# Optimization experiments

Measured on AMD Instinct MI355X. Metric: run time of the kernel, lower is better.

Reference implementation:

```python
import jax, jax.numpy as jnp
import numpy as np

N_NODES = 50000


def sage_conv(x, src, dst, Wl, bl, Wr):
    # mean-aggregate neighbor features: message from src -> dst
    msg = x[src]                                            # [E, d]
    agg = jax.ops.segment_sum(msg, dst, num_segments=N_NODES)
    deg = jax.ops.segment_sum(jnp.ones((src.shape[0],), x.dtype), dst,
                              num_segments=N_NODES)
    mean = agg / jnp.clip(deg, 1.0)[:, None]                # [N, d]
    # PyG SAGEConv: lin_l(mean) + lin_r(x); lin_l has bias, lin_r does not
    return mean @ Wl.T + bl + x @ Wr.T


def setup_inputs() -> dict:
    key = jax.random.key(0)
    ks = jax.random.split(key, 10)
    d_in, d_h = 128, 256
    E = 800000
    x = jax.random.normal(ks[0], (N_NODES, d_in), jnp.float32)
    edge_index = jax.random.randint(ks[1], (2, E), 0, N_NODES, jnp.int32)
    s = 0.05
    return {
        "x": x,
        "edge_index": edge_index,
        "W1_l": jax.random.normal(ks[2], (d_h, d_in), jnp.float32) * s,
        "b1": jax.random.normal(ks[3], (d_h,), jnp.float32) * s,
        "W1_r": jax.random.normal(ks[4], (d_h, d_in), jnp.float32) * s,
        "W2_l": jax.random.normal(ks[5], (d_h, d_h), jnp.float32) * s,
        "b2": jax.random.normal(ks[6], (d_h,), jnp.float32) * s,
        "W2_r": jax.random.normal(ks[7], (d_h, d_h), jnp.float32) * s,
        "head_w": jax.random.normal(ks[8], (1, d_h), jnp.float32) * s,
        "head_b": jax.random.normal(ks[9], (1,), jnp.float32) * s,
    }


def reference(x, edge_index, W1_l, b1, W1_r, W2_l, b2, W2_r, head_w, head_b):
    src, dst = edge_index[0], edge_index[1]
    h = jax.nn.relu(sage_conv(x, src, dst, W1_l, b1, W1_r))
    # dropout is identity in eval mode
    h = jax.nn.relu(sage_conv(h, src, dst, W2_l, b2, W2_r))
    out = h @ head_w.T + head_b                              # [N, 1]
    return out[:, 0]                                         # [N]
```

## Files before the change

kernel.cpp:

```cpp
#include <hip/hip_runtime.h>
#include <hip/hip_bf16.h>

#define D_IN 128
#define D_H  256

typedef __attribute__((ext_vector_type(8))) short short8;
typedef __attribute__((ext_vector_type(4))) float floatx4;

__device__ __forceinline__ unsigned short f2bf(float f) {
    __hip_bfloat16 h = __float2bfloat16(f);
    return *reinterpret_cast<unsigned short*>(&h);
}
__device__ __forceinline__ float bf2f(unsigned short s) {
    union { unsigned int u; float f; } v;
    v.u = ((unsigned int)s) << 16;
    return v.f;
}

__global__ void hist_conv_k(const int* __restrict__ dst, int* __restrict__ deg,
                            int* __restrict__ rank, int E,
                            const float* __restrict__ x, unsigned short* __restrict__ xb, int nx4,
                            const float* __restrict__ w1l, unsigned short* __restrict__ w1lb,
                            const float* __restrict__ w1r, unsigned short* __restrict__ w1rb, int nw14,
                            const float* __restrict__ w2l, unsigned short* __restrict__ w2lb,
                            const float* __restrict__ w2r, unsigned short* __restrict__ w2rb, int nw24) {
    if (blockIdx.x < 512) {
        for (int e = blockIdx.x * 256 + threadIdx.x; e < E; e += 512 * 256)
            rank[e] = atomicAdd(&deg[dst[e]], 1);
        return;
    }
    int i = (blockIdx.x - 512) * 256 + threadIdx.x;
    const float* s; unsigned short* d; int k;
    if (i < nx4) { s = x; d = xb; k = i; }
    else {
        i -= nx4;
        if (i < nw14) { s = w1l; d = w1lb; k = i; }
        else {
            i -= nw14;
            if (i < nw14) { s = w1r; d = w1rb; k = i; }
            else {
                i -= nw14;
                if (i < nw24) { s = w2l; d = w2lb; k = i; }
                else {
                    i -= nw24;
                    if (i >= nw24) return;
                    s = w2r; d = w2rb; k = i;
                }
            }
        }
    }
    float4 v = ((const float4*)s)[k];
    ushort4 u;
    u.x = f2bf(v.x); u.y = f2bf(v.y); u.z = f2bf(v.z); u.w = f2bf(v.w);
    ((ushort4*)d)[k] = u;
}

__global__ __launch_bounds__(256) void scan_part_k(const int* __restrict__ deg,
                                                   int* __restrict__ bsum, int n) {
    const int b = blockIdx.x, tid = threadIdx.x;
    const int base = b * 2048;
    const int lim = min(base + 2048, n);
    int s = 0;
    for (int i = base + tid; i < lim; i += 256) s += deg[i];
    __shared__ int red[256];
    red[tid] = s; __syncthreads();
    for (int off = 128; off > 0; off >>= 1) {
        if (tid < off) red[tid] += red[tid + off];
        __syncthreads();
    }
    if (tid == 0) bsum[b] = red[0];
}

__global__ __launch_bounds__(256) void scan_final_k(const int* __restrict__ deg,
                                                    const int* __restrict__ bsum,
                                                    int* __restrict__ row_ptr,
                                                    int n, int E) {
    const int b = blockIdx.x, tid = threadIdx.x;
    const int base = b * 2048;
    __shared__ int buf[2048];
    __shared__ int ts[256];
    __shared__ int blk_prefix;
    if (tid == 0) {
        int p = 0;
        for (int i = 0; i < b; ++i) p += bsum[i];
        blk_prefix = p;
    }
    for (int i = tid; i < 2048; i += 256)
        buf[i] = (base + i < n) ? deg[base + i] : 0;
    __syncthreads();
    int local[8];
    int s = 0;
#pragma unroll
    for (int j = 0; j < 8; ++j) { local[j] = s; s += buf[tid * 8 + j]; }
    ts[tid] = s; __syncthreads();
    for (int off = 1; off < 256; off <<= 1) {
        int v = (tid >= off) ? ts[tid - off] : 0;
        __syncthreads();
        ts[tid] += v;
        __syncthreads();
    }
    const int prefix = blk_prefix + ((tid == 0) ? 0 : ts[tid - 1]);
#pragma unroll
    for (int j = 0; j < 8; ++j) {
        int idx = base + tid * 8 + j;
        if (idx < n) row_ptr[idx] = prefix + local[j];
    }
    if (b == 0 && tid == 0) row_ptr[n] = E;
}

__global__ void scatter_k(const int* __restrict__ src, const int* __restrict__ dst,
                          const int* __restrict__ rank, const int* __restrict__ row_ptr,
                          int* __restrict__ col, int E) {
    for (int e = blockIdx.x * blockDim.x + threadIdx.x; e < E; e += gridDim.x * blockDim.x)
        col[row_ptr[dst[e]] + rank[e]] = src[e];
}

template <int D, int UN>
__device__ __forceinline__ int agg_stage(const unsigned short* __restrict__ X,
                                         const int* __restrict__ col,
                                         int j, int e, int lane, float* acc) {
    constexpr int V = D / 64;
    for (; j + UN <= e; j += UN) {
        int cs[UN];
#pragma unroll
        for (int u = 0; u < UN; ++u) cs[u] = col[j + u];
        if constexpr (V == 2) {
            unsigned int vals[UN];
#pragma unroll
            for (int u = 0; u < UN; ++u)
                vals[u] = *(const unsigned int*)(X + (size_t)cs[u] * D + lane * 2);
#pragma unroll
            for (int u = 0; u < UN; ++u) {
                acc[0] += bf2f((unsigned short)(vals[u] & 0xffff));
                acc[1] += bf2f((unsigned short)(vals[u] >> 16));
            }
        } else {
            ushort4 vals[UN];
#pragma unroll
            for (int u = 0; u < UN; ++u)
                vals[u] = *(const ushort4*)(X + (size_t)cs[u] * D + lane * 4);
#pragma unroll
            for (int u = 0; u < UN; ++u) {
                acc[0] += bf2f(vals[u].x); acc[1] += bf2f(vals[u].y);
                acc[2] += bf2f(vals[u].z); acc[3] += bf2f(vals[u].w);
            }
        }
    }
    return j;
}

template <int D>
__global__ __launch_bounds__(256) void aggregate_v3(
    const unsigned short* __restrict__ X, const int* __restrict__ col,
    const int* __restrict__ rp, unsigned short* __restrict__ out, int Mnodes) {
    int node = __builtin_amdgcn_readfirstlane((blockIdx.x << 2) + (threadIdx.x >> 6));
    if (node >= Mnodes) return;
    const int lane = threadIdx.x & 63;
    const int s = rp[node], e = rp[node + 1];
    constexpr int V = D / 64;
    float acc[V] = {0.f};

    int j = s;
    j = agg_stage<D, 8>(X, col, j, e, lane, acc);
    j = agg_stage<D, 4>(X, col, j, e, lane, acc);
    j = agg_stage<D, 2>(X, col, j, e, lane, acc);
    j = agg_stage<D, 1>(X, col, j, e, lane, acc);

    const float inv = 1.f / fmaxf((float)(e - s), 1.f);
    if constexpr (V == 2) {
        ushort2 o;
        o.x = f2bf(acc[0] * inv); o.y = f2bf(acc[1] * inv);
        *(ushort2*)(out + (size_t)node * D + lane * 2) = o;
    } else {
        ushort4 o;
        o.x = f2bf(acc[0] * inv); o.y = f2bf(acc[1] * inv);
        o.z = f2bf(acc[2] * inv); o.w = f2bf(acc[3] * inv);
        *(ushort4*)(out + (size_t)node * D + lane * 4) = o;
    }
}

template <int K, bool HEAD>
__global__ __launch_bounds__(256, 2) void gemm_mfma_k(
    const unsigned short* __restrict__ A1, const unsigned short* __restrict__ W1,
    const unsigned short* __restrict__ A2, const unsigned short* __restrict__ W2,
    const float* __restrict__ bias, unsigned short* __restrict__ Hout,
    const float* __restrict__ hw, const float* __restrict__ hb,
    float* __restrict__ out, int M) {
    __shared__ __align__(16) unsigned short sA[128 * 40];
    __shared__ __align__(16) unsigned short sB[256 * 40];
    __shared__ float head_acc[128];

    const int tid = threadIdx.x;
    const int wave = tid >> 6;
    const int lane = tid & 63;
    const int c = lane & 15;
    const int q = lane >> 4;
    const int m0 = blockIdx.x * 128;

    if (HEAD && tid < 128) head_acc[tid] = 0.f;

    floatx4 acc[8][4];
#pragma unroll
    for (int mi = 0; mi < 8; ++mi)
#pragma unroll
        for (int ni = 0; ni < 4; ++ni) acc[mi][ni] = (floatx4){0.f, 0.f, 0.f, 0.f};

    const int arow = tid >> 1;
    const int aseg = (tid & 1) * 16;
    const int brow = tid >> 2;
    const int bseg = (tid & 3) * 8;
    int gr = m0 + arow;
    if (gr >= M) gr = M - 1;

    for (int phase = 0; phase < 2; ++phase) {
        const unsigned short* Ap = phase ? A2 : A1;
        const unsigned short* Wp = phase ? W2 : W1;
        for (int k0 = 0; k0 < K; k0 += 32) {
            short8 va0 = *(const short8*)(Ap + (size_t)gr * K + k0 + aseg);
            short8 va1 = *(const short8*)(Ap + (size_t)gr * K + k0 + aseg + 8);
            short8 vb[4];
#pragma unroll
            for (int i = 0; i < 4; ++i)
                vb[i] = *(const short8*)(Wp + (size_t)(brow + i * 64) * K + k0 + bseg);
            __syncthreads();
            *(short8*)&sA[arow * 40 + aseg] = va0;
            *(short8*)&sA[arow * 40 + aseg + 8] = va1;
#pragma unroll
            for (int i = 0; i < 4; ++i)
                *(short8*)&sB[(brow + i * 64) * 40 + bseg] = vb[i];
            __syncthreads();

            short8 af[8], bf[4];
#pragma unroll
            for (int mi = 0; mi < 8; ++mi)
                af[mi] = *(const short8*)&sA[(mi * 16 + c) * 40 + q * 8];
#pragma unroll
            for (int ni = 0; ni < 4; ++ni)
                bf[ni] = *(const short8*)&sB[(wave * 64 + ni * 16 + c) * 40 + q * 8];
#pragma unroll
            for (int mi = 0; mi < 8; ++mi)
#pragma unroll
                for (int ni = 0; ni < 4; ++ni)
                    acc[mi][ni] = __builtin_amdgcn_mfma_f32_16x16x32_bf16(
                        af[mi], bf[ni], acc[mi][ni], 0, 0, 0);
        }
    }

    if (!HEAD) {
#pragma unroll
        for (int mi = 0; mi < 8; ++mi)
#pragma unroll
            for (int ni = 0; ni < 4; ++ni) {
                const int n = wave * 64 + ni * 16 + c;
                const float bv = bias[n];
#pragma unroll
                for (int reg = 0; reg < 4; ++reg) {
                    const int m = m0 + mi * 16 + q * 4 + reg;
                    if (m < M) {
                        float v = fmaxf(acc[mi][ni][reg] + bv, 0.f);
                        Hout[(size_t)m * 256 + n] = f2bf(v);
                    }
                }
            }
    } else {
#pragma unroll
        for (int mi = 0; mi < 8; ++mi) {
            float p[4] = {0.f, 0.f, 0.f, 0.f};
#pragma unroll
            for (int ni = 0; ni < 4; ++ni) {
                const int n = wave * 64 + ni * 16 + c;
                const float bv = bias[n];
                const float hv = hw[n];
#pragma unroll
                for (int reg = 0; reg < 4; ++reg)
                    p[reg] += fmaxf(acc[mi][ni][reg] + bv, 0.f) * hv;
            }
#pragma unroll
            for (int reg = 0; reg < 4; ++reg) {
                float v = p[reg];
                v += __shfl_xor(v, 1, 64);
                v += __shfl_xor(v, 2, 64);
                v += __shfl_xor(v, 4, 64);
                v += __shfl_xor(v, 8, 64);
                if (c == 0) atomicAdd(&head_acc[mi * 16 + q * 4 + reg], v);
            }
        }
        __syncthreads();
        if (tid < 128) {
            const int m = m0 + tid;
            if (m < M) out[m] = head_acc[tid] + hb[0];
        }
    }
}

extern "C" void kernel_launch(void* const* d_in, const int* in_sizes, int n_in,
                              void* d_out, int out_size, void* d_ws, size_t ws_size,
                              hipStream_t stream) {
    const float* x    = (const float*)d_in[0];
    const int*   ei   = (const int*)d_in[1];
    const float* W1l  = (const float*)d_in[2];
    const float* b1   = (const float*)d_in[3];
    const float* W1r  = (const float*)d_in[4];
    const float* W2l  = (const float*)d_in[5];
    const float* b2   = (const float*)d_in[6];
    const float* W2r  = (const float*)d_in[7];
    const float* hw   = (const float*)d_in[8];
    const float* hb   = (const float*)d_in[9];
    float* out = (float*)d_out;

    const int M = in_sizes[0] / D_IN;
    const int E = in_sizes[1] / 2;
    const int* src = ei;
    const int* dst = ei + E;

    size_t off = 0;
    auto alloc = [&](size_t bytes) -> void* {
        void* p = (char*)d_ws + off;
        off += (bytes + 255) & ~(size_t)255;
        return p;
    };
    int* deg  = (int*)alloc((size_t)M * 4);
    int* rp   = (int*)alloc((size_t)(M + 1) * 4);
    int* bsum = (int*)alloc(256 * 4);
    int* rank = (int*)alloc((size_t)E * 4);
    int* col  = (int*)alloc((size_t)E * 4);
    unsigned short* xb    = (unsigned short*)alloc((size_t)M * D_IN * 2);
    unsigned short* w1lb  = (unsigned short*)alloc((size_t)D_H * D_IN * 2);
    unsigned short* w1rb  = (unsigned short*)alloc((size_t)D_H * D_IN * 2);
    unsigned short* w2lb  = (unsigned short*)alloc((size_t)D_H * D_H * 2);
    unsigned short* w2rb  = (unsigned short*)alloc((size_t)D_H * D_H * 2);
    unsigned short* mean1 = (unsigned short*)alloc((size_t)M * D_IN * 2);
    unsigned short* h1    = (unsigned short*)alloc((size_t)M * D_H * 2);
    unsigned short* mean2 = (unsigned short*)alloc((size_t)M * D_H * 2);

    hipMemsetAsync(deg, 0, (size_t)M * 4, stream);

    const int nx4 = (M * D_IN) / 4;
    const int nw14 = (D_H * D_IN) / 4;
    const int nw24 = (D_H * D_H) / 4;
    const int tot4 = nx4 + 2 * nw14 + 2 * nw24;
    const int convblk = (tot4 + 255) / 256;
    hist_conv_k<<<512 + convblk, 256, 0, stream>>>(
        dst, deg, rank, E,
        x, xb, nx4, W1l, w1lb, W1r, w1rb, nw14, W2l, w2lb, W2r, w2rb, nw24);

    const int nseg = (M + 2047) / 2048;
    scan_part_k<<<nseg, 256, 0, stream>>>(deg, bsum, M);
    scan_final_k<<<nseg, 256, 0, stream>>>(deg, bsum, rp, M, E);
    scatter_k<<<512, 256, 0, stream>>>(src, dst, rank, rp, col, E);

    const int nblk = (M + 127) / 128;
    const int ablk = (M + 3) / 4;

    aggregate_v3<D_IN><<<ablk, 256, 0, stream>>>(xb, col, rp, mean1, M);
    gemm_mfma_k<D_IN, false><<<nblk, 256, 0, stream>>>(
        mean1, w1lb, xb, w1rb, b1, h1, nullptr, nullptr, nullptr, M);

    aggregate_v3<D_H><<<ablk, 256, 0, stream>>>(h1, col, rp, mean2, M);
    gemm_mfma_k<D_H, true><<<nblk, 256, 0, stream>>>(
        mean2, w2lb, h1, w2rb, b2, nullptr, hw, hb, out, M);
}
```

Baseline: 270.2 us.

## Split 128-dim aggregation across half-waves and fold scan into one kernel

The D=128 aggregation now has each half-wave take alternate edges, loading 8 bytes per lane instead of 4, and combines the two halves with a cross-lane shuffle. The D=256 path drops its 8-wide unroll stage. The separate partial-sum scan kernel is removed; each scan block now re-reduces all preceding degrees itself, which saves one launch but makes later blocks read more data. The new half-wave split needs extra tail handling and a shuffle reduction.

```diff
diff --git a/kernel.cpp b/kernel.cpp
--- a/kernel.cpp
+++ b/kernel.cpp
@@ -55,24 +55,7 @@
     ((ushort4*)d)[k] = u;
 }
 
-__global__ __launch_bounds__(256) void scan_part_k(const int* __restrict__ deg,
-                                                   int* __restrict__ bsum, int n) {
-    const int b = blockIdx.x, tid = threadIdx.x;
-    const int base = b * 2048;
-    const int lim = min(base + 2048, n);
-    int s = 0;
-    for (int i = base + tid; i < lim; i += 256) s += deg[i];
-    __shared__ int red[256];
-    red[tid] = s; __syncthreads();
-    for (int off = 128; off > 0; off >>= 1) {
-        if (tid < off) red[tid] += red[tid + off];
-        __syncthreads();
-    }
-    if (tid == 0) bsum[b] = red[0];
-}
-
 __global__ __launch_bounds__(256) void scan_final_k(const int* __restrict__ deg,
-                                                    const int* __restrict__ bsum,
                                                     int* __restrict__ row_ptr,
                                                     int n, int E) {
     const int b = blockIdx.x, tid = threadIdx.x;
@@ -80,11 +63,17 @@
     __shared__ int buf[2048];
     __shared__ int ts[256];
     __shared__ int blk_prefix;
-    if (tid == 0) {
-        int p = 0;
-        for (int i = 0; i < b; ++i) p += bsum[i];
-        blk_prefix = p;
-    }
+
+    int pre = 0;
+    for (int i = tid; i < base; i += 256) pre += deg[i];
+    ts[tid] = pre; __syncthreads();
+    for (int off = 128; off > 0; off >>= 1) {
+        if (tid < off) ts[tid] += ts[tid + off];
+        __syncthreads();
+    }
+    if (tid == 0) blk_prefix = ts[0];
+    __syncthreads();
+
     for (int i = tid; i < 2048; i += 256)
         buf[i] = (base + i < n) ? deg[base + i] : 0;
     __syncthreads();
@@ -115,67 +104,92 @@
         col[row_ptr[dst[e]] + rank[e]] = src[e];
 }
 
-template <int D, int UN>
-__device__ __forceinline__ int agg_stage(const unsigned short* __restrict__ X,
-                                         const int* __restrict__ col,
-                                         int j, int e, int lane, float* acc) {
-    constexpr int V = D / 64;
+template <int UN>
+__device__ __forceinline__ int agg_stage256(const unsigned short* __restrict__ X,
+                                            const int* __restrict__ col,
+                                            int j, int e, int lane, float* acc) {
     for (; j + UN <= e; j += UN) {
         int cs[UN];
 #pragma unroll
         for (int u = 0; u < UN; ++u) cs[u] = col[j + u];
-        if constexpr (V == 2) {
-            unsigned int vals[UN];
-#pragma unroll
-            for (int u = 0; u < UN; ++u)
-                vals[u] = *(const unsigned int*)(X + (size_t)cs[u] * D + lane * 2);
-#pragma unroll
-            for (int u = 0; u < UN; ++u) {
-                acc[0] += bf2f((unsigned short)(vals[u] & 0xffff));
-                acc[1] += bf2f((unsigned short)(vals[u] >> 16));
-            }
-        } else {
-            ushort4 vals[UN];
-#pragma unroll
-            for (int u = 0; u < UN; ++u)
-                vals[u] = *(const ushort4*)(X + (size_t)cs[u] * D + lane * 4);
-#pragma unroll
-            for (int u = 0; u < UN; ++u) {
-                acc[0] += bf2f(vals[u].x); acc[1] += bf2f(vals[u].y);
-                acc[2] += bf2f(vals[u].z); acc[3] += bf2f(vals[u].w);
-            }
+        ushort4 vals[UN];
+#pragma unroll
+        for (int u = 0; u < UN; ++u)
+            vals[u] = *(const ushort4*)(X + (size_t)cs[u] * 256 + lane * 4);
+#pragma unroll
+        for (int u = 0; u < UN; ++u) {
+            acc[0] += bf2f(vals[u].x); acc[1] += bf2f(vals[u].y);
+            acc[2] += bf2f(vals[u].z); acc[3] += bf2f(vals[u].w);
         }
     }
     return j;
 }
 
+template <int UN>
+__device__ __forceinline__ int agg_stage128(const unsigned short* __restrict__ X,
+                                            const int* __restrict__ col,
+                                            int j, int e, int half, int l16, float* acc) {
+    for (; j + 2 * UN <= e; j += 2 * UN) {
+        int cs[UN];
+#pragma unroll
+        for (int u = 0; u < UN; ++u) cs[u] = col[j + 2 * u + half];
+        ushort4 vals[UN];
+#pragma unroll
+        for (int u = 0; u < UN; ++u)
+            vals[u] = *(const ushort4*)(X + (size_t)cs[u] * 128 + l16 * 4);
+#pragma unroll
+        for (int u = 0; u < UN; ++u) {
+            acc[0] += bf2f(vals[u].x); acc[1] += bf2f(vals[u].y);
+            acc[2] += bf2f(vals[u].z); acc[3] += bf2f(vals[u].w);
+        }
+    }
+    return j;
+}
+
 template <int D>
-__global__ __launch_bounds__(256) void aggregate_v3(
+__global__ __launch_bounds__(256) void aggregate_v4(
     const unsigned short* __restrict__ X, const int* __restrict__ col,
     const int* __restrict__ rp, unsigned short* __restrict__ out, int Mnodes) {
     int node = __builtin_amdgcn_readfirstlane((blockIdx.x << 2) + (threadIdx.x >> 6));
     if (node >= Mnodes) return;
     const int lane = threadIdx.x & 63;
     const int s = rp[node], e = rp[node + 1];
-    constexpr int V = D / 64;
-    float acc[V] = {0.f};
-
-    int j = s;
-    j = agg_stage<D, 8>(X, col, j, e, lane, acc);
-    j = agg_stage<D, 4>(X, col, j, e, lane, acc);
-    j = agg_stage<D, 2>(X, col, j, e, lane, acc);
-    j = agg_stage<D, 1>(X, col, j, e, lane, acc);
-
-    const float inv = 1.f / fmaxf((float)(e - s), 1.f);
-    if constexpr (V == 2) {
-        ushort2 o;
-        o.x = f2bf(acc[0] * inv); o.y = f2bf(acc[1] * inv);
-        *(ushort2*)(out + (size_t)node * D + lane * 2) = o;
-    } else {
+    float acc[4] = {0.f, 0.f, 0.f, 0.f};
+
+    if constexpr (D == 256) {
+        int j = s;
+        j = agg_stage256<4>(X, col, j, e, lane, acc);
+        j = agg_stage256<2>(X, col, j, e, lane, acc);
+        j = agg_stage256<1>(X, col, j, e, lane, acc);
+        const float inv = 1.f / fmaxf((float)(e - s), 1.f);
         ushort4 o;
         o.x = f2bf(acc[0] * inv); o.y = f2bf(acc[1] * inv);
         o.z = f2bf(acc[2] * inv); o.w = f2bf(acc[3] * inv);
-        *(ushort4*)(out + (size_t)node * D + lane * 4) = o;
+        *(ushort4*)(out + (size_t)node * 256 + lane * 4) = o;
+    } else {
+        const int half = lane >> 5;
+        const int l16 = lane & 31;
+        int j = s;
+        j = agg_stage128<4>(X, col, j, e, half, l16, acc);
+        j = agg_stage128<2>(X, col, j, e, half, l16, acc);
+        j = agg_stage128<1>(X, col, j, e, half, l16, acc);
+        if (j < e) {
+            int c0 = col[j];
+            const ushort4 v = *(const ushort4*)(X + (size_t)c0 * 128 + l16 * 4);
+            if (half == 0) {
+                acc[0] += bf2f(v.x); acc[1] += bf2f(v.y);
+                acc[2] += bf2f(v.z); acc[3] += bf2f(v.w);
+            }
+        }
+#pragma unroll
+        for (int k = 0; k < 4; ++k) acc[k] += __shfl_xor(acc[k], 32, 64);
+        const float inv = 1.f / fmaxf((float)(e - s), 1.f);
+        if (half == 0) {
+            ushort4 o;
+            o.x = f2bf(acc[0] * inv); o.y = f2bf(acc[1] * inv);
+            o.z = f2bf(acc[2] * inv); o.w = f2bf(acc[3] * inv);
+            *(ushort4*)(out + (size_t)node * 128 + l16 * 4) = o;
+        }
     }
 }
 
@@ -321,7 +335,6 @@
     };
     int* deg  = (int*)alloc((size_t)M * 4);
     int* rp   = (int*)alloc((size_t)(M + 1) * 4);
-    int* bsum = (int*)alloc(256 * 4);
     int* rank = (int*)alloc((size_t)E * 4);
     int* col  = (int*)alloc((size_t)E * 4);
     unsigned short* xb    = (unsigned short*)alloc((size_t)M * D_IN * 2);
@@ -345,18 +358,17 @@
         x, xb, nx4, W1l, w1lb, W1r, w1rb, nw14, W2l, w2lb, W2r, w2rb, nw24);
 
     const int nseg = (M + 2047) / 2048;
-    scan_part_k<<<nseg, 256, 0, stream>>>(deg, bsum, M);
-    scan_final_k<<<nseg, 256, 0, stream>>>(deg, bsum, rp, M, E);
+    scan_final_k<<<nseg, 256, 0, stream>>>(deg, rp, M, E);
     scatter_k<<<512, 256, 0, stream>>>(src, dst, rank, rp, col, E);
 
     const int nblk = (M + 127) / 128;
     const int ablk = (M + 3) / 4;
 
-    aggregate_v3<D_IN><<<ablk, 256, 0, stream>>>(xb, col, rp, mean1, M);
+    aggregate_v4<D_IN><<<ablk, 256, 0, stream>>>(xb, col, rp, mean1, M);
     gemm_mfma_k<D_IN, false><<<nblk, 256, 0, stream>>>(
         mean1, w1lb, xb, w1rb, b1, h1, nullptr, nullptr, nullptr, M);
 
-    aggregate_v3<D_H><<<ablk, 256, 0, stream>>>(h1, col, rp, mean2, M);
+    aggregate_v4<D_H><<<ablk, 256, 0, stream>>>(h1, col, rp, mean2, M);
     gemm_mfma_k<D_H, true><<<nblk, 256, 0, stream>>>(
         mean2, w2lb, h1, w2rb, b2, nullptr, hw, hb, out, M);
 }
```

New measurement: 294.9 us. 1.09x slower.

## Load GEMM tiles directly into LDS with global_load_lds and XOR swizzle

Applied to the files above, without the earlier changes.

Replaces the register-staged global-to-LDS copy in the MFMA GEMM with direct global_load_lds transfers of 16 bytes per lane. The padded LDS rows (stride 40) become unpadded rows of 32, with an XOR swizzle on the 8-element segment index to avoid bank conflicts on the fragment reads. The launch bound's minimum-occupancy hint is dropped. This aims to cut register pressure and VGPR round-trips on the load path, but the loop is still single-buffered, with syncs around each stage, so load latency is not overlapped with compute.

```diff
diff --git a/kernel.cpp b/kernel.cpp
--- a/kernel.cpp
+++ b/kernel.cpp
@@ -180,14 +180,14 @@
 }
 
 template <int K, bool HEAD>
-__global__ __launch_bounds__(256, 2) void gemm_mfma_k(
+__global__ __launch_bounds__(256) void gemm_mfma_k(
     const unsigned short* __restrict__ A1, const unsigned short* __restrict__ W1,
     const unsigned short* __restrict__ A2, const unsigned short* __restrict__ W2,
     const float* __restrict__ bias, unsigned short* __restrict__ Hout,
     const float* __restrict__ hw, const float* __restrict__ hb,
     float* __restrict__ out, int M) {
-    __shared__ __align__(16) unsigned short sA[128 * 40];
-    __shared__ __align__(16) unsigned short sB[256 * 40];
+    __shared__ __align__(16) unsigned short sA[128 * 32];
+    __shared__ __align__(16) unsigned short sB[256 * 32];
     __shared__ float head_acc[128];
 
     const int tid = threadIdx.x;
@@ -205,38 +205,47 @@
 #pragma unroll
         for (int ni = 0; ni < 4; ++ni) acc[mi][ni] = (floatx4){0.f, 0.f, 0.f, 0.f};
 
-    const int arow = tid >> 1;
-    const int aseg = (tid & 1) * 16;
-    const int brow = tid >> 2;
-    const int bseg = (tid & 3) * 8;
-    int gr = m0 + arow;
-    if (gr >= M) gr = M - 1;
+    int aRow[2], aSegU[2], gA[2];
+#pragma unroll
+    for (int j = 0; j < 2; ++j) {
+        const int L = j * 256 + tid;
+        aRow[j] = L >> 2;
+        aSegU[j] = ((L & 3) ^ ((aRow[j] >> 1) & 3)) * 8;
+        gA[j] = min(m0 + aRow[j], M - 1);
+    }
+    int bRow[4], bSegU[4];
+#pragma unroll
+    for (int j = 0; j < 4; ++j) {
+        const int L = j * 256 + tid;
+        bRow[j] = L >> 2;
+        bSegU[j] = ((L & 3) ^ ((bRow[j] >> 1) & 3)) * 8;
+    }
+    const int sc = (q ^ ((c >> 1) & 3)) * 8;
 
     for (int phase = 0; phase < 2; ++phase) {
         const unsigned short* Ap = phase ? A2 : A1;
         const unsigned short* Wp = phase ? W2 : W1;
         for (int k0 = 0; k0 < K; k0 += 32) {
-            short8 va0 = *(const short8*)(Ap + (size_t)gr * K + k0 + aseg);
-            short8 va1 = *(const short8*)(Ap + (size_t)gr * K + k0 + aseg + 8);
-            short8 vb[4];
-#pragma unroll
-            for (int i = 0; i < 4; ++i)
-                vb[i] = *(const short8*)(Wp + (size_t)(brow + i * 64) * K + k0 + bseg);
             __syncthreads();
-            *(short8*)&sA[arow * 40 + aseg] = va0;
-            *(short8*)&sA[arow * 40 + aseg + 8] = va1;
-#pragma unroll
-            for (int i = 0; i < 4; ++i)
-                *(short8*)&sB[(brow + i * 64) * 40 + bseg] = vb[i];
+#pragma unroll
+            for (int j = 0; j < 2; ++j)
+                __builtin_amdgcn_global_load_lds(
+                    (const unsigned int*)(Ap + (size_t)gA[j] * K + k0 + aSegU[j]),
+                    (unsigned int*)&sA[(j * 256 + wave * 64) * 8], 16, 0, 0);
+#pragma unroll
+            for (int j = 0; j < 4; ++j)
+                __builtin_amdgcn_global_load_lds(
+                    (const unsigned int*)(Wp + (size_t)bRow[j] * K + k0 + bSegU[j]),
+                    (unsigned int*)&sB[(j * 256 + wave * 64) * 8], 16, 0, 0);
             __syncthreads();
 
             short8 af[8], bf[4];
 #pragma unroll
             for (int mi = 0; mi < 8; ++mi)
-                af[mi] = *(const short8*)&sA[(mi * 16 + c) * 40 + q * 8];
+                af[mi] = *(const short8*)&sA[(mi * 16 + c) * 32 + sc];
 #pragma unroll
             for (int ni = 0; ni < 4; ++ni)
-                bf[ni] = *(const short8*)&sB[(wave * 64 + ni * 16 + c) * 40 + q * 8];
+                bf[ni] = *(const short8*)&sB[(wave * 64 + ni * 16 + c) * 32 + sc];
 #pragma unroll
             for (int mi = 0; mi < 8; ++mi)
 #pragma unroll
```

Result: slower. 303.6 us (+12.4%).
